# Performance work log

Measured on AMD Instinct MI355X. Metric: run time of the kernel, lower is better.

## Reference

```python
import jax, jax.numpy as jnp
import numpy as np

LAYER_VEC = [2000, 200, 100, 10]
EN_DIMS = [(2000, 200), (200, 100), (100, 10)]      # (num_in, num_out) per encoder FC_layer
DE_DIMS = [(10, 100), (100, 200), (200, 2000)]      # decoder is reversed
EN_SIZES = [ni * no + no for ni, no in EN_DIMS]     # [400200, 20100, 1010] -> 421310
DE_SIZES = [ni * no + no for ni, no in DE_DIMS]     # [1100, 20200, 402000] -> 423300
ACT_VEC = ['linear', 'tanh', 'linear']              # ['linear'] + (len-3)*[activation] + ['linear']


def _hyper(mu, W0, b0, W1, b1, W2, b2):
    # nn.Sequential: Linear -> tanh -> Linear -> tanh -> Linear (depth_hyper=2)
    h = jnp.tanh(mu @ W0.T + b0)
    h = jnp.tanh(h @ W1.T + b1)
    return h @ W2.T + b2  # [B, param_size]


def _fc_layer(x, p, num_in, num_out):
    # FC_layer.forward: per-sample weight matvec + bias
    B = x.shape[0]
    w = p[:, :num_out * num_in].reshape(B, num_out, num_in)
    b = p[:, num_out * num_in:]
    return jnp.einsum('ab,acb->ac', x, w) + b


def _act(x, name):
    return jnp.tanh(x) if name == 'tanh' else x


def _run_stack(data, params, dims, sizes):
    cut = 0
    for (ni, no), sz, a in zip(dims, sizes, ACT_VEC):
        data = _act(_fc_layer(data, params[:, cut:cut + sz], ni, no), a)
        cut += sz
    return data


def setup_inputs() -> dict:
    key = jax.random.key(0)
    ks = jax.random.split(key, 16)
    B, NS, W = 64, 4, 64
    EN_P, DE_P = sum(EN_SIZES), sum(DE_SIZES)
    f32 = jnp.float32
    inp = {
        'z':  jax.random.normal(ks[0], (B, LAYER_VEC[0]), f32),
        'mu': jax.random.normal(ks[1], (B, NS), f32),
        'en_W0': jax.random.normal(ks[2], (W, NS), f32) / np.sqrt(NS),
        'en_b0': jnp.zeros((W,), f32),
        'en_W1': jax.random.normal(ks[3], (W, W), f32) / np.sqrt(W),
        'en_b1': jnp.zeros((W,), f32),
        'en_W2': jax.random.normal(ks[4], (EN_P, W), f32) * 0.01,
        'en_b2': jnp.zeros((EN_P,), f32),
        'de_W0': jax.random.normal(ks[5], (W, NS), f32) / np.sqrt(NS),
        'de_b0': jnp.zeros((W,), f32),
        'de_W1': jax.random.normal(ks[6], (W, W), f32) / np.sqrt(W),
        'de_b1': jnp.zeros((W,), f32),
        'de_W2': jax.random.normal(ks[7], (DE_P, W), f32) * 0.01,
        'de_b2': jnp.zeros((DE_P,), f32),
    }
    return inp


def reference(z, mu, en_W0, en_b0, en_W1, en_b1, en_W2, en_b2,
              de_W0, de_b0, de_W1, de_b1, de_W2, de_b2):
    # encode
    p_en = _hyper(mu, en_W0, en_b0, en_W1, en_b1, en_W2, en_b2)
    x = _run_stack(z, p_en, EN_DIMS, EN_SIZES)
    # decode
    p_de = _hyper(mu, de_W0, de_b0, de_W1, de_b1, de_W2, de_b2)
    z_reconst = _run_stack(x, p_de, DE_DIMS, DE_SIZES)
    return (z_reconst, x)
```

## Files before the change

### kernel.cpp

```cpp
#include <hip/hip_runtime.h>


__global__ __launch_bounds__(256) void prep_kernel(
    const float* __restrict__ z, const float* __restrict__ mu,
    const float* __restrict__ enW0, const float* __restrict__ enb0,
    const float* __restrict__ enW1, const float* __restrict__ enb1,
    const float* __restrict__ deW0, const float* __restrict__ deb0,
    const float* __restrict__ deW1, const float* __restrict__ deb1,
    float* __restrict__ zT, float* __restrict__ hen, float* __restrict__ hde)
{
    __shared__ float tile[64 * 65];
    __shared__ float h0s[4][64];
    const int bid  = blockIdx.x;
    const int lane = threadIdx.x & 63;
    const int g    = threadIdx.x >> 6;

    if (bid < 32) {
        const int t0 = bid * 64;
        for (int bb = g; bb < 64; bb += 4) {
            int i = t0 + lane;
            tile[bb * 65 + lane] = (i < 2000) ? z[bb * 2000 + i] : 0.f;
        }
        __syncthreads();
        for (int ii = g; ii < 64; ii += 4) {
            int i = t0 + ii;
            if (i < 2000) zT[i * 64 + lane] = tile[lane * 65 + ii];
        }
    } else {
        const int task  = (bid - 32) * 4 + g;
        const int which = task >> 6;
        const int b     = task & 63;
        const float* W0 = which ? deW0 : enW0;
        const float* b0 = which ? deb0 : enb0;
        const float* W1 = which ? deW1 : enW1;
        const float* b1 = which ? deb1 : enb1;
        float* hout     = which ? hde : hen;
        const int j = lane;
        float m0 = mu[b * 4 + 0], m1 = mu[b * 4 + 1], m2 = mu[b * 4 + 2], m3 = mu[b * 4 + 3];
        float v = tanhf(m0 * W0[j * 4 + 0] + m1 * W0[j * 4 + 1] +
                        m2 * W0[j * 4 + 2] + m3 * W0[j * 4 + 3] + b0[j]);
        h0s[g][j] = v;
        __syncthreads();
        float a = b1[j];
        const float* W1r = W1 + j * 64;
        #pragma unroll 8
        for (int k = 0; k < 64; ++k) a = fmaf(h0s[g][k], W1r[k], a);
        hout[b * 64 + j] = tanhf(a);
    }
}

template <int NI, int NO, int NSPLIT, bool TANH, bool ATOMIC>
__global__ __launch_bounds__(256, 2) void fc_kernel(
    const float* __restrict__ xT,
    const float* __restrict__ h,
    const float* __restrict__ W2,
    const float* __restrict__ b2,
    float* __restrict__ yT)
{
    __shared__ float R[2][64 * 64];
    __shared__ float xbs[256];
    const int lane = threadIdx.x & 63;
    const int wave = __builtin_amdgcn_readfirstlane(threadIdx.x >> 6);
    const int o = blockIdx.x / NSPLIT;
    const int s = blockIdx.x % NSPLIT;
    constexpr int CH = NI / NSPLIT;
    const int i0 = s * CH;
    const int iend = i0 + CH;

    const float* __restrict__ Wbase = W2 + (size_t)o * NI * 64;
    const float* __restrict__ b2w   = b2 + (size_t)o * NI;

    float acc[64];
    #pragma unroll
    for (int b = 0; b < 64; ++b) acc[b] = 0.f;
    float xb_acc = 0.f;

    #pragma unroll 2
    for (int i = i0 + wave; i < iend; i += 4) {
        float w = Wbase[(size_t)i * 64 + lane];
        float xv_l = xT[i * 64 + lane];
        xb_acc = fmaf(xv_l, b2w[i], xb_acc);
        const float4* xr = (const float4*)(xT + i * 64);
        #pragma unroll
        for (int q = 0; q < 16; ++q) {
            float4 xv = xr[q];
            acc[4 * q + 0] = fmaf(xv.x, w, acc[4 * q + 0]);
            acc[4 * q + 1] = fmaf(xv.y, w, acc[4 * q + 1]);
            acc[4 * q + 2] = fmaf(xv.z, w, acc[4 * q + 2]);
            acc[4 * q + 3] = fmaf(xv.w, w, acc[4 * q + 3]);
        }
    }

    xbs[wave * 64 + lane] = xb_acc;

    if (wave == 1) {
        #pragma unroll
        for (int b = 0; b < 64; ++b) R[0][b * 64 + lane] = acc[b];
    } else if (wave == 3) {
        #pragma unroll
        for (int b = 0; b < 64; ++b) R[1][b * 64 + lane] = acc[b];
    }
    __syncthreads();
    if (wave == 0) {
        #pragma unroll
        for (int b = 0; b < 64; ++b) acc[b] += R[0][b * 64 + lane];
    } else if (wave == 2) {
        #pragma unroll
        for (int b = 0; b < 64; ++b) acc[b] += R[1][b * 64 + lane];
    }
    __syncthreads();
    if (wave == 0) {
        #pragma unroll
        for (int b = 0; b < 64; ++b) R[0][b * 64 + lane] = acc[b];
    } else if (wave == 2) {
        #pragma unroll
        for (int b = 0; b < 64; ++b) R[1][b * 64 + lane] = acc[b];
    }
    __syncthreads();

    float wsel = 0.f;
    if (!ATOMIC || s == 0) wsel = W2[((size_t)NO * NI + o) * 64 + lane];
    float myv = 0.f;
    #pragma unroll
    for (int j = 0; j < 16; ++j) {
        int b = wave * 16 + j;
        float t = R[0][b * 64 + lane] + R[1][b * 64 + lane];
        float v = (t + wsel) * h[b * 64 + lane];
        #pragma unroll
        for (int m = 32; m >= 1; m >>= 1) v += __shfl_xor(v, m, 64);
        if (lane == j) myv = v;
    }
    if (lane < 16) {
        int b = wave * 16 + lane;
        float xbt = xbs[b] + xbs[64 + b] + xbs[128 + b] + xbs[192 + b];
        float out = myv + xbt;
        if (!ATOMIC || s == 0) out += b2[(size_t)NO * NI + o];
        if (TANH) out = tanhf(out);
        if (ATOMIC) atomicAdd(&yT[o * 64 + b], out);
        else        yT[o * 64 + b] = out;
    }
}

__global__ __launch_bounds__(256) void final_kernel(
    const float* __restrict__ d3,
    const float* __restrict__ y3,
    float* __restrict__ out)
{
    int t = blockIdx.x * 256 + threadIdx.x;
    if (t < 128000) {
        int b = t / 2000, oo = t - b * 2000;
        out[t] = d3[oo * 64 + b];
    } else if (t < 128640) {
        int u = t - 128000;
        int b = u / 10, oo = u - b * 10;
        out[t] = y3[oo * 64 + b];
    }
}

extern "C" void kernel_launch(void* const* d_in, const int* in_sizes, int n_in,
                              void* d_out, int out_size, void* d_ws, size_t ws_size,
                              hipStream_t stream)
{
    const float* z    = (const float*)d_in[0];
    const float* mu   = (const float*)d_in[1];
    const float* enW0 = (const float*)d_in[2];
    const float* enb0 = (const float*)d_in[3];
    const float* enW1 = (const float*)d_in[4];
    const float* enb1 = (const float*)d_in[5];
    const float* enW2 = (const float*)d_in[6];
    const float* enb2 = (const float*)d_in[7];
    const float* deW0 = (const float*)d_in[8];
    const float* deb0 = (const float*)d_in[9];
    const float* deW1 = (const float*)d_in[10];
    const float* deb1 = (const float*)d_in[11];
    const float* deW2 = (const float*)d_in[12];
    const float* deb2 = (const float*)d_in[13];

    float* ws  = (float*)d_ws;
    float* zT  = ws;
    float* hen = zT + 128000;
    float* hde = hen + 4096;
    float* y1  = hde + 4096;
    float* y2  = y1 + 200 * 64;
    float* y3  = y2 + 100 * 64;
    float* d1  = y3 + 10 * 64;
    float* d2  = d1 + 100 * 64;
    float* d3  = d2 + 200 * 64;
    float* out = (float*)d_out;

    hipMemsetAsync(y1, 0, 200 * 64 * sizeof(float), stream);
    prep_kernel<<<64, 256, 0, stream>>>(z, mu, enW0, enb0, enW1, enb1,
                                        deW0, deb0, deW1, deb1, zT, hen, hde);
    fc_kernel<2000, 200, 8, false, true ><<<1600, 256, 0, stream>>>(zT, hen, enW2, enb2, y1);
    fc_kernel< 200, 100, 1, true,  false><<< 100, 256, 0, stream>>>(y1, hen, enW2 + (size_t)400200 * 64, enb2 + 400200, y2);
    fc_kernel< 100,  10, 1, false, false><<<  10, 256, 0, stream>>>(y2, hen, enW2 + (size_t)420300 * 64, enb2 + 420300, y3);
    fc_kernel<  10, 100, 1, false, false><<< 100, 256, 0, stream>>>(y3, hde, deW2, deb2, d1);
    fc_kernel< 100, 200, 1, true,  false><<< 200, 256, 0, stream>>>(d1, hde, deW2 + (size_t)1100 * 64, deb2 + 1100, d2);
    fc_kernel< 200, 2000, 1, false, false><<<2000, 256, 0, stream>>>(d2, hde, deW2 + (size_t)21300 * 64, deb2 + 21300, d3);

    final_kernel<<<(128640 + 255) / 256, 256, 0, stream>>>(d3, y3, out);
}
```

Measured before the change: 382.5 us.

## Retile fc_kernel into per-thread 4x4 register blocks without shared-memory reduction

The per-block work is re-partitioned so each thread holds a 4x4 tile (4 batch rows by 4 hyper-weight columns), replacing the 64-register accumulator and the cross-wave shared-memory reduction. Each wave now walks the whole input chunk for its own 16 batch rows using float4 loads of W2 and xT, and reduces over the hyper dimension with 16-lane shuffles. Launch bounds are raised to allow more blocks per CU, and the block index mapping is swapped so split chunks of the same output are spread apart. The trade-off is that every wave streams the full W2 chunk, so weight loads are repeated four times per block, though they should mostly hit in cache.

```diff
diff --git a/kernel.cpp b/kernel.cpp
--- a/kernel.cpp
+++ b/kernel.cpp
@@ -50,94 +50,117 @@
 }
 
 template <int NI, int NO, int NSPLIT, bool TANH, bool ATOMIC>
-__global__ __launch_bounds__(256, 2) void fc_kernel(
+__global__ __launch_bounds__(256, 8) void fc_kernel(
     const float* __restrict__ xT,
     const float* __restrict__ h,
     const float* __restrict__ W2,
     const float* __restrict__ b2,
     float* __restrict__ yT)
 {
-    __shared__ float R[2][64 * 64];
-    __shared__ float xbs[256];
     const int lane = threadIdx.x & 63;
-    const int wave = __builtin_amdgcn_readfirstlane(threadIdx.x >> 6);
-    const int o = blockIdx.x / NSPLIT;
-    const int s = blockIdx.x % NSPLIT;
+    const int wave = threadIdx.x >> 6;
+    const int kg   = lane & 15;
+    const int bgl  = lane >> 4;
+    const int b0   = wave * 16 + bgl * 4;
+
+    const int o = blockIdx.x % NO;
+    const int s = blockIdx.x / NO;
     constexpr int CH = NI / NSPLIT;
-    const int i0 = s * CH;
+    const int i0   = s * CH;
     const int iend = i0 + CH;
 
-    const float* __restrict__ Wbase = W2 + (size_t)o * NI * 64;
-    const float* __restrict__ b2w   = b2 + (size_t)o * NI;
-
-    float acc[64];
+    const float* __restrict__ Wp = W2 + ((size_t)o * NI + i0) * 64 + 4 * kg;
+    const float* __restrict__ xp = xT + (size_t)i0 * 64 + b0;
+
+    float acc[4][4];
     #pragma unroll
-    for (int b = 0; b < 64; ++b) acc[b] = 0.f;
-    float xb_acc = 0.f;
+    for (int a = 0; a < 4; ++a)
+        #pragma unroll
+        for (int c = 0; c < 4; ++c) acc[a][c] = 0.f;
 
     #pragma unroll 2
-    for (int i = i0 + wave; i < iend; i += 4) {
-        float w = Wbase[(size_t)i * 64 + lane];
-        float xv_l = xT[i * 64 + lane];
-        xb_acc = fmaf(xv_l, b2w[i], xb_acc);
-        const float4* xr = (const float4*)(xT + i * 64);
-        #pragma unroll
-        for (int q = 0; q < 16; ++q) {
-            float4 xv = xr[q];
-            acc[4 * q + 0] = fmaf(xv.x, w, acc[4 * q + 0]);
-            acc[4 * q + 1] = fmaf(xv.y, w, acc[4 * q + 1]);
-            acc[4 * q + 2] = fmaf(xv.z, w, acc[4 * q + 2]);
-            acc[4 * q + 3] = fmaf(xv.w, w, acc[4 * q + 3]);
-        }
-    }
-
-    xbs[wave * 64 + lane] = xb_acc;
-
-    if (wave == 1) {
-        #pragma unroll
-        for (int b = 0; b < 64; ++b) R[0][b * 64 + lane] = acc[b];
-    } else if (wave == 3) {
-        #pragma unroll
-        for (int b = 0; b < 64; ++b) R[1][b * 64 + lane] = acc[b];
-    }
-    __syncthreads();
-    if (wave == 0) {
-        #pragma unroll
-        for (int b = 0; b < 64; ++b) acc[b] += R[0][b * 64 + lane];
-    } else if (wave == 2) {
-        #pragma unroll
-        for (int b = 0; b < 64; ++b) acc[b] += R[1][b * 64 + lane];
-    }
-    __syncthreads();
-    if (wave == 0) {
-        #pragma unroll
-        for (int b = 0; b < 64; ++b) R[0][b * 64 + lane] = acc[b];
-    } else if (wave == 2) {
-        #pragma unroll
-        for (int b = 0; b < 64; ++b) R[1][b * 64 + lane] = acc[b];
-    }
-    __syncthreads();
-
-    float wsel = 0.f;
-    if (!ATOMIC || s == 0) wsel = W2[((size_t)NO * NI + o) * 64 + lane];
-    float myv = 0.f;
+    for (int i = i0; i < iend; ++i) {
+        const float4 w = *(const float4*)Wp;  Wp += 64;
+        const float4 x = *(const float4*)xp;  xp += 64;
+        {
+            const float xa = x.x;
+            acc[0][0] = fmaf(xa, w.x, acc[0][0]);
+            acc[0][1] = fmaf(xa, w.y, acc[0][1]);
+            acc[0][2] = fmaf(xa, w.z, acc[0][2]);
+            acc[0][3] = fmaf(xa, w.w, acc[0][3]);
+        }
+        {
+            const float xa = x.y;
+            acc[1][0] = fmaf(xa, w.x, acc[1][0]);
+            acc[1][1] = fmaf(xa, w.y, acc[1][1]);
+            acc[1][2] = fmaf(xa, w.z, acc[1][2]);
+            acc[1][3] = fmaf(xa, w.w, acc[1][3]);
+        }
+        {
+            const float xa = x.z;
+            acc[2][0] = fmaf(xa, w.x, acc[2][0]);
+            acc[2][1] = fmaf(xa, w.y, acc[2][1]);
+            acc[2][2] = fmaf(xa, w.z, acc[2][2]);
+            acc[2][3] = fmaf(xa, w.w, acc[2][3]);
+        }
+        {
+            const float xa = x.w;
+            acc[3][0] = fmaf(xa, w.x, acc[3][0]);
+            acc[3][1] = fmaf(xa, w.y, acc[3][1]);
+            acc[3][2] = fmaf(xa, w.z, acc[3][2]);
+            acc[3][3] = fmaf(xa, w.w, acc[3][3]);
+        }
+    }
+
+    const float* __restrict__ b2w = b2 + (size_t)o * NI;
+    float xb[4] = {0.f, 0.f, 0.f, 0.f};
+    constexpr int T16 = (CH + 15) / 16;
+    #pragma unroll 4
+    for (int t = 0; t < T16; ++t) {
+        const int ib = i0 + t * 16 + kg;
+        if (ib < iend) {
+            const float  bv = b2w[ib];
+            const float4 xq = *(const float4*)(xT + (size_t)ib * 64 + b0);
+            xb[0] = fmaf(xq.x, bv, xb[0]);
+            xb[1] = fmaf(xq.y, bv, xb[1]);
+            xb[2] = fmaf(xq.z, bv, xb[2]);
+            xb[3] = fmaf(xq.w, bv, xb[3]);
+        }
+    }
+
+    float4 wb = make_float4(0.f, 0.f, 0.f, 0.f);
+    if (!ATOMIC || s == 0)
+        wb = *(const float4*)(W2 + ((size_t)NO * NI + o) * 64 + 4 * kg);
+
+    float out0, out1, out2, out3;
     #pragma unroll
-    for (int j = 0; j < 16; ++j) {
-        int b = wave * 16 + j;
-        float t = R[0][b * 64 + lane] + R[1][b * 64 + lane];
-        float v = (t + wsel) * h[b * 64 + lane];
-        #pragma unroll
-        for (int m = 32; m >= 1; m >>= 1) v += __shfl_xor(v, m, 64);
-        if (lane == j) myv = v;
-    }
-    if (lane < 16) {
-        int b = wave * 16 + lane;
-        float xbt = xbs[b] + xbs[64 + b] + xbs[128 + b] + xbs[192 + b];
-        float out = myv + xbt;
-        if (!ATOMIC || s == 0) out += b2[(size_t)NO * NI + o];
-        if (TANH) out = tanhf(out);
-        if (ATOMIC) atomicAdd(&yT[o * 64 + b], out);
-        else        yT[o * 64 + b] = out;
+    for (int a = 0; a < 4; ++a) {
+        const float4 hv = *(const float4*)(h + (size_t)(b0 + a) * 64 + 4 * kg);
+        float v = xb[a];
+        v = fmaf(hv.x, acc[a][0] + wb.x, v);
+        v = fmaf(hv.y, acc[a][1] + wb.y, v);
+        v = fmaf(hv.z, acc[a][2] + wb.z, v);
+        v = fmaf(hv.w, acc[a][3] + wb.w, v);
+        v += __shfl_xor(v, 1, 64);
+        v += __shfl_xor(v, 2, 64);
+        v += __shfl_xor(v, 4, 64);
+        v += __shfl_xor(v, 8, 64);
+        if (a == 0) out0 = v;
+        else if (a == 1) out1 = v;
+        else if (a == 2) out2 = v;
+        else out3 = v;
+    }
+
+    if (kg < 4) {
+        float v = out0;
+        v = (kg == 1) ? out1 : v;
+        v = (kg == 2) ? out2 : v;
+        v = (kg == 3) ? out3 : v;
+        const int b = b0 + kg;
+        if (!ATOMIC || s == 0) v += b2[(size_t)NO * NI + o];
+        if (TANH) v = tanhf(v);
+        if (ATOMIC) atomicAdd(&yT[o * 64 + b], v);
+        else        yT[o * 64 + b] = v;
     }
 }
 
```

Result: slower. 623.8 us (+63.1%).

## Split FC kernel work across waves by batch slice instead of input rows

Applied to the files above, without the earlier changes.

Each wave now owns 16 batch columns and loops over every input row in the chunk, so it keeps 16 accumulators instead of 64. This removes the shared-memory cross-wave reduction and its three barriers. The lower register use lets launch bounds rise to 8 blocks per SM. The block index mapping also changes so that split chunks of the same output are spread across the grid. The trade-off is that all four waves now read the same weight row, giving four times the redundant weight loads, which should mostly be served from cache.

```diff
diff --git a/kernel.cpp b/kernel.cpp
--- a/kernel.cpp
+++ b/kernel.cpp
@@ -50,40 +50,37 @@
 }
 
 template <int NI, int NO, int NSPLIT, bool TANH, bool ATOMIC>
-__global__ __launch_bounds__(256, 2) void fc_kernel(
+__global__ __launch_bounds__(256, 8) void fc_kernel(
     const float* __restrict__ xT,
     const float* __restrict__ h,
     const float* __restrict__ W2,
     const float* __restrict__ b2,
     float* __restrict__ yT)
 {
-    __shared__ float R[2][64 * 64];
-    __shared__ float xbs[256];
     const int lane = threadIdx.x & 63;
     const int wave = __builtin_amdgcn_readfirstlane(threadIdx.x >> 6);
-    const int o = blockIdx.x / NSPLIT;
-    const int s = blockIdx.x % NSPLIT;
+    const int b0   = wave * 16;
+
+    const int o = blockIdx.x % NO;
+    const int s = blockIdx.x / NO;
     constexpr int CH = NI / NSPLIT;
-    const int i0 = s * CH;
+    const int i0   = s * CH;
     const int iend = i0 + CH;
 
-    const float* __restrict__ Wbase = W2 + (size_t)o * NI * 64;
-    const float* __restrict__ b2w   = b2 + (size_t)o * NI;
+    const float* __restrict__ Wp = W2 + ((size_t)o * NI + i0) * 64 + lane;
+    const float* __restrict__ xp = xT + (size_t)i0 * 64 + b0;
 
-    float acc[64];
+    float acc[16];
     #pragma unroll
-    for (int b = 0; b < 64; ++b) acc[b] = 0.f;
-    float xb_acc = 0.f;
+    for (int j = 0; j < 16; ++j) acc[j] = 0.f;
 
-    #pragma unroll 2
-    for (int i = i0 + wave; i < iend; i += 4) {
-        float w = Wbase[(size_t)i * 64 + lane];
-        float xv_l = xT[i * 64 + lane];
-        xb_acc = fmaf(xv_l, b2w[i], xb_acc);
-        const float4* xr = (const float4*)(xT + i * 64);
+    #pragma unroll 4
+    for (int i = i0; i < iend; ++i) {
+        const float w = *Wp;  Wp += 64;
+        const float4* xr = (const float4*)xp;  xp += 64;
         #pragma unroll
-        for (int q = 0; q < 16; ++q) {
-            float4 xv = xr[q];
+        for (int q = 0; q < 4; ++q) {
+            const float4 xv = xr[q];
             acc[4 * q + 0] = fmaf(xv.x, w, acc[4 * q + 0]);
             acc[4 * q + 1] = fmaf(xv.y, w, acc[4 * q + 1]);
             acc[4 * q + 2] = fmaf(xv.z, w, acc[4 * q + 2]);
@@ -91,49 +88,30 @@
         }
     }
 
-    xbs[wave * 64 + lane] = xb_acc;
+    const float* __restrict__ b2w = b2 + (size_t)o * NI;
+    float xbp = 0.f;
+    for (int i = i0 + (lane >> 4); i < iend; i += 4) {
+        xbp = fmaf(xT[(size_t)i * 64 + b0 + (lane & 15)], b2w[i], xbp);
+    }
+    xbp += __shfl_xor(xbp, 16, 64);
+    xbp += __shfl_xor(xbp, 32, 64);
 
-    if (wave == 1) {
-        #pragma unroll
-        for (int b = 0; b < 64; ++b) R[0][b * 64 + lane] = acc[b];
-    } else if (wave == 3) {
-        #pragma unroll
-        for (int b = 0; b < 64; ++b) R[1][b * 64 + lane] = acc[b];
-    }
-    __syncthreads();
-    if (wave == 0) {
-        #pragma unroll
-        for (int b = 0; b < 64; ++b) acc[b] += R[0][b * 64 + lane];
-    } else if (wave == 2) {
-        #pragma unroll
-        for (int b = 0; b < 64; ++b) acc[b] += R[1][b * 64 + lane];
-    }
-    __syncthreads();
-    if (wave == 0) {
-        #pragma unroll
-        for (int b = 0; b < 64; ++b) R[0][b * 64 + lane] = acc[b];
-    } else if (wave == 2) {
-        #pragma unroll
-        for (int b = 0; b < 64; ++b) R[1][b * 64 + lane] = acc[b];
-    }
-    __syncthreads();
+    float wbv = 0.f;
+    if (!ATOMIC || s == 0) wbv = W2[((size_t)NO * NI + o) * 64 + lane];
 
-    float wsel = 0.f;
-    if (!ATOMIC || s == 0) wsel = W2[((size_t)NO * NI + o) * 64 + lane];
     float myv = 0.f;
     #pragma unroll
     for (int j = 0; j < 16; ++j) {
-        int b = wave * 16 + j;
-        float t = R[0][b * 64 + lane] + R[1][b * 64 + lane];
-        float v = (t + wsel) * h[b * 64 + lane];
+        const int b = b0 + j;
+        float v = (acc[j] + wbv) * h[(size_t)b * 64 + lane];
         #pragma unroll
         for (int m = 32; m >= 1; m >>= 1) v += __shfl_xor(v, m, 64);
         if (lane == j) myv = v;
     }
+
     if (lane < 16) {
-        int b = wave * 16 + lane;
-        float xbt = xbs[b] + xbs[64 + b] + xbs[128 + b] + xbs[192 + b];
-        float out = myv + xbt;
+        const int b = b0 + lane;
+        float out = myv + xbp;
         if (!ATOMIC || s == 0) out += b2[(size_t)NO * NI + o];
         if (TANH) out = tanhf(out);
         if (ATOMIC) atomicAdd(&yT[o * 64 + b], out);
```

After: 477.9 us. 1.25x slower.
